# Kernel optimization log

Measured on AMD Instinct MI355X. Metric: run time of the kernel, lower is better.

Reference implementation:

```python
import jax, jax.numpy as jnp
import numpy as np

EPS = 1e-8


def l2norm(x, axis):
    # matches torch: x / (sqrt(sum(x^2)) + eps)
    return x / (jnp.sqrt(jnp.sum(x * x, axis=axis, keepdims=True)) + EPS)


def setup_inputs() -> dict:
    key = jax.random.key(0)
    k1, k2, k3, k4, k5 = jax.random.split(key, 5)
    I, C, L, R, D = 16, 32, 32, 36, 1024  # n_image, n_caption, max_words, n_regions, embed_dim
    img_emb = l2norm(jax.random.normal(k1, (I, R, D), jnp.float32), -1)
    cap_emb = l2norm(jax.random.normal(k2, (C, L, D), jnp.float32), -1)
    W_emb = jax.random.normal(k3, (D, D), jnp.float32)  # nn.Embedding weight, N(0,1) default init
    sim_map_w = 2.5 + 0.1 * jax.random.normal(k4, (1, D), jnp.float32)  # init_weight: normal(2.5, 0.1)
    temp_scale_w = jnp.full((1, 1), np.log(1.0 / 0.07), jnp.float32)    # init_weight
    temp_learnable_w = jnp.full((1, 1), 4.0, jnp.float32)               # init_weight
    cap_lens = jax.random.randint(k5, (C,), 4, L + 1, jnp.int32)        # ragged caption lengths in [4, L]
    return dict(img_emb=img_emb, cap_emb=cap_emb, W_emb=W_emb, sim_map_w=sim_map_w,
                temp_scale_w=temp_scale_w, temp_learnable_w=temp_learnable_w, cap_lens=cap_lens)


def reference(img_emb, cap_emb, W_emb, sim_map_w, temp_scale_w, temp_learnable_w, cap_lens):
    D = W_emb.shape[0]
    L = cap_emb.shape[1]
    # --- dimension-weight branch (caption-independent) ---
    # linspace(0, D, D).long(): last index is D (out of range in torch); gather with clip.
    idx = jnp.floor(jnp.linspace(0.0, D, D)).astype(jnp.int32)
    weights = jax.nn.sigmoid(jnp.take(W_emb, idx, axis=0, mode='clip'))  # (D, D)
    mean_p = jnp.mean(weights, axis=1)                  # (D,)
    std_p = jnp.std(weights, axis=1, ddof=1)            # torch.std is unbiased
    thres = mean_p + sim_map_w[0] * std_p               # (D,)
    values = jnp.exp(temp_learnable_w[0, 0]) * (weights - thres[:, None])
    mask_p = jnp.tanh(jnp.exp(values))
    Dlw = l2norm(mask_p * weights, axis=1)              # Dim_learned_weights (D, D)
    diag = Dlw.sum(0)                                   # Diagonal (D,); diag_embed matmul == elementwise scale
    smooth = jnp.exp(temp_scale_w[0, 0])
    # --- vectorized ragged per-caption cross attention ---
    wmask = (jnp.arange(L)[None, :] < cap_lens[:, None]).astype(cap_emb.dtype)  # (C, L)
    # attn[c,i,l,r] = tanh(sum_d cap[c,l,d] * diag[d] * img[i,r,d])
    attn = jnp.tanh(jnp.einsum('cld,ird->cilr', cap_emb, img_emb * diag))
    attn = jnp.where(attn >= 0, attn, 0.1 * attn) * wmask[:, None, :, None]  # LeakyReLU(0.1), zero padded words
    attn = attn / (jnp.sqrt(jnp.sum(attn * attn, axis=2, keepdims=True)) + EPS)  # l2norm over word dim
    attn = jax.nn.softmax(attn * smooth, axis=3)        # softmax over regions
    ctx = l2norm(jnp.einsum('cilr,ird->cild', attn, img_emb), axis=-1)  # Context_img
    sim_loc = ctx * cap_emb[:, None, :, :]
    sim_sub = jnp.einsum('cild,ed->cile', sim_loc, Dlw)  # sim_loc @ Dlw.T
    sim_vec = l2norm(sim_sub, axis=-1).sum(-1)           # (C, I, L)
    # mean over the n_word valid words of each caption
    sim = jnp.sum(sim_vec * wmask[:, None, :], axis=2) / cap_lens[:, None].astype(cap_emb.dtype)  # (C, I)
    return sim.T  # (n_image, n_caption), matching torch.cat(sim_all, 1)
```

## Files before the change

kernel.cpp:

```cpp
#include <hip/hip_runtime.h>
#include <hip/hip_bf16.h>

#define I_N 16
#define C_N 32
#define L_N 32
#define R_N 36
#define D_N 1024
#define EPSF 1e-8f

typedef _Float16 f16;
typedef __attribute__((ext_vector_type(8))) _Float16 half8;
typedef __attribute__((ext_vector_type(4))) float floatx4;

__device__ __forceinline__ void gl16(const f16* g, f16* l) {
  __builtin_amdgcn_global_load_lds(
      (const __attribute__((address_space(1))) void*)g,
      (__attribute__((address_space(3))) void*)l, 16, 0, 0);
}

__device__ __forceinline__ float fast_tanh(float x) {
  float q = __expf(-2.f * fabsf(x));
  float t = (1.f - q) / (1.f + q);
  return (x >= 0.f) ? t : -t;
}

__device__ __forceinline__ float wave_sum64(float v) {
  #pragma unroll
  for (int off = 32; off > 0; off >>= 1) v += __shfl_xor(v, off, 64);
  return v;
}

__global__ __launch_bounds__(256) void k_dlw(const float* __restrict__ W,
    const float* __restrict__ simw, const float* __restrict__ tlw,
    const float* __restrict__ img,
    f16* __restrict__ DlwH, f16* __restrict__ imgP) {
  int gw = blockIdx.x * 4 + (threadIdx.x >> 6);
  int lane = threadIdx.x & 63;
  if (gw >= 1024) {
    int row = gw - 1024;
    int i = row / 48, r = row % 48;
    size_t dst = (size_t)row * D_N;
    #pragma unroll
    for (int q = 0; q < 4; ++q) {
      int col = lane * 4 + q * 256;
      f16 h4[4];
      if (r < R_N) {
        size_t src = ((size_t)i * R_N + r) * D_N;
        float4 v = *(const float4*)(img + src + col);
        h4[0] = (f16)v.x; h4[1] = (f16)v.y; h4[2] = (f16)v.z; h4[3] = (f16)v.w;
      } else {
        h4[0] = h4[1] = h4[2] = h4[3] = (f16)0.f;
      }
      *(float2*)(imgP + dst + col) = *(float2*)h4;
    }
    return;
  }
  int row = gw;
  const float* Wr = W + (size_t)row * D_N;
  float w[16]; float p = 0.f;
  #pragma unroll
  for (int q = 0; q < 4; ++q) {
    float4 v = *(const float4*)(Wr + lane * 4 + q * 256);
    w[q*4+0] = 1.f / (1.f + __expf(-v.x));
    w[q*4+1] = 1.f / (1.f + __expf(-v.y));
    w[q*4+2] = 1.f / (1.f + __expf(-v.z));
    w[q*4+3] = 1.f / (1.f + __expf(-v.w));
    p += w[q*4+0] + w[q*4+1] + w[q*4+2] + w[q*4+3];
  }
  float S = wave_sum64(p);
  float mean = S * (1.f / 1024.f);
  p = 0.f;
  #pragma unroll
  for (int k = 0; k < 16; ++k) { float d = w[k] - mean; p += d * d; }
  float S2 = wave_sum64(p);
  float stdv = sqrtf(S2 * (1.f / 1023.f));
  float thres = mean + simw[row] * stdv;
  float eT = __expf(tlw[0]);
  p = 0.f;
  #pragma unroll
  for (int k = 0; k < 16; ++k) {
    float y = __expf(eT * (w[k] - thres));
    float q2 = __expf(-2.f * y);
    float mp = (1.f - q2) / (1.f + q2);
    w[k] = mp * w[k];
    p += w[k] * w[k];
  }
  float S3 = wave_sum64(p);
  float inv = 1.f / (sqrtf(S3) + EPSF);
  #pragma unroll
  for (int q = 0; q < 4; ++q) {
    f16 h4[4];
    #pragma unroll
    for (int t = 0; t < 4; ++t) h4[t] = (f16)(w[q*4+t] * inv);
    *(float2*)(DlwH + (size_t)row * D_N + lane * 4 + q * 256) = *(float2*)h4;
  }
}

__global__ __launch_bounds__(256) void k_dpp(const f16* __restrict__ DlwH,
    const int* __restrict__ lens, float* __restrict__ dpart,
    int* __restrict__ pfx, int* __restrict__ mp) {
  int bid = blockIdx.x;
  if (bid < 64) {
    int p = bid >> 2;
    int col = (bid & 3) * 256 + threadIdx.x;
    float s = 0.f;
    #pragma unroll 8
    for (int r = p * 64; r < p * 64 + 64; ++r) s += (float)DlwH[(size_t)r * D_N + col];
    dpart[(size_t)p * D_N + col] = s;
  } else if (threadIdx.x < 64) {
    int l = threadIdx.x;
    int v = (l < 32) ? lens[l] : 0;
    int s = v;
    #pragma unroll
    for (int off = 1; off < 32; off <<= 1) {
      int t = __shfl_up(s, off, 64);
      if (l >= off) s += t;
    }
    if (l < 32) pfx[l] = s - v;
    if (l == 31) { pfx[32] = s; mp[0] = s * 16; }
  }
}

__global__ __launch_bounds__(256) void k_capd(const float* __restrict__ dpart,
    const float* __restrict__ cap, f16* __restrict__ capD) {
  __shared__ float dg[D_N];
  int tid = threadIdx.x;
  #pragma unroll
  for (int k = 0; k < 4; ++k) {
    int col = tid + k * 256;
    float s = 0.f;
    #pragma unroll
    for (int p = 0; p < 16; ++p) s += dpart[(size_t)p * D_N + col];
    dg[col] = s;
  }
  __syncthreads();
  #pragma unroll
  for (int rr = 0; rr < 4; ++rr) {
    size_t base = (size_t)(blockIdx.x * 4 + rr) * D_N;
    #pragma unroll
    for (int k = 0; k < 4; ++k) {
      int j = tid + k * 256;
      capD[base + j] = (f16)(cap[base + j] * dg[j]);
    }
  }
}

__global__ __launch_bounds__(256) void k_qk(const f16* __restrict__ A,
    const f16* __restrict__ B, const int* __restrict__ lens,
    const float* __restrict__ tsw, float* __restrict__ pw) {
  int mt = blockIdx.x;
  int i  = blockIdx.y;
  int tid = threadIdx.x;
  int w = tid >> 6, lane = tid & 63;
  int l15 = lane & 15, h = lane >> 4;
  __shared__ __align__(16) f16 Abuf[3][64 * 32];
  __shared__ __align__(16) f16 Bbuf[3][64 * 32];
  __shared__ float att[64][49];
  __shared__ float cn[2][R_N];
  floatx4 acc[3];
  #pragma unroll
  for (int nf = 0; nf < 3; ++nf) acc[nf] = (floatx4)0.f;

  int r_p = lane >> 2, u_p = lane & 3;
  int sw = (r_p >> 1) & 7;
  int val = (u_p | ((r_p & 1) << 2)) ^ sw;
  int r_l = (r_p & 14) | (val >> 2);
  int u_l = val & 3;
  const f16* Ag = A + (size_t)(mt * 64 + w * 16 + r_l) * D_N + u_l * 8;
  const f16* Bg = B + (size_t)(i * 48 + w * 16 + r_l) * D_N + u_l * 8;

  int v2 = (h | ((l15 & 1) << 2)) ^ ((l15 >> 1) & 7);
  int rbit = (v2 >> 2) & 1;
  int pun = (v2 & 3) * 8;
  int aoff = (w * 16 + (l15 & 14) + rbit) * 32 + pun;
  int boff[3];
  #pragma unroll
  for (int nf = 0; nf < 3; ++nf) boff[nf] = (nf * 16 + (l15 & 14) + rbit) * 32 + pun;

  #define QSTAGE(kt, b) { \
    int kof = (kt) * 32; \
    gl16(Ag + kof, &Abuf[b][(w * 16) * 32]); \
    gl16(Bg + kof, &Bbuf[b][(w * 16) * 32]); }
  #define QCOMPUTE(b) { \
    half8 a = *(const half8*)(&Abuf[b][aoff]); \
    _Pragma("unroll") for (int nf = 0; nf < 3; ++nf) { \
      half8 bb = *(const half8*)(&Bbuf[b][boff[nf]]); \
      acc[nf] = __builtin_amdgcn_mfma_f32_16x16x32_f16(a, bb, acc[nf], 0, 0, 0); } }

  QSTAGE(0, 0);
  QSTAGE(1, 1);
  int cur = 0, n2 = 2;
  for (int kk = 0; kk < 30; ++kk) {
    QSTAGE(kk + 2, n2);
    asm volatile("s_waitcnt vmcnt(4)" ::: "memory");
    __builtin_amdgcn_s_barrier();
    __builtin_amdgcn_sched_barrier(0);
    QCOMPUTE(cur);
    __builtin_amdgcn_s_barrier();
    cur = (cur == 2) ? 0 : cur + 1;
    n2  = (n2  == 2) ? 0 : n2  + 1;
  }
  asm volatile("s_waitcnt vmcnt(2)" ::: "memory");
  __builtin_amdgcn_s_barrier();
  __builtin_amdgcn_sched_barrier(0);
  QCOMPUTE(cur);
  __builtin_amdgcn_s_barrier();
  cur = (cur == 2) ? 0 : cur + 1;
  asm volatile("s_waitcnt vmcnt(0)" ::: "memory");
  __builtin_amdgcn_s_barrier();
  __builtin_amdgcn_sched_barrier(0);
  QCOMPUTE(cur);
  #undef QSTAGE
  #undef QCOMPUTE

  int len0 = lens[mt * 2], len1 = lens[mt * 2 + 1];
  #pragma unroll
  for (int nf = 0; nf < 3; ++nf)
    #pragma unroll
    for (int j = 0; j < 4; ++j) {
      int ml = w * 16 + h * 4 + j;
      int n = nf * 16 + l15;
      float t = fast_tanh(acc[nf][j]);
      float v = (t >= 0.f) ? t : 0.1f * t;
      int len = (ml >= 32) ? len1 : len0;
      if ((ml & 31) >= len || n >= R_N) v = 0.f;
      att[ml][n] = v;
    }
  __syncthreads();
  for (int e = tid; e < 2 * R_N; e += 256) {
    int cc = e / R_N, r = e % R_N;
    float s = 0.f;
    #pragma unroll
    for (int l = 0; l < 32; ++l) { float a = att[cc * 32 + l][r]; s += a * a; }
    cn[cc][r] = sqrtf(s) + EPSF;
  }
  __syncthreads();
  if (tid < 64) {
    int cc = tid >> 5, l = tid & 31;
    float smooth = __expf(tsw[0]);
    float mx = -3.4e38f;
    #pragma unroll
    for (int r = 0; r < R_N; ++r) {
      float z = att[tid][r] / cn[cc][r] * smooth;
      att[tid][r] = z;
      mx = fmaxf(mx, z);
    }
    float se = 0.f;
    #pragma unroll
    for (int r = 0; r < R_N; ++r) {
      float e2 = __expf(att[tid][r] - mx);
      att[tid][r] = e2;
      se += e2;
    }
    float inv = 1.f / se;
    float* dst = pw + ((size_t)i * 1024 + (mt * 2 + cc) * 32 + l) * R_N;
    #pragma unroll
    for (int r = 0; r < R_N; ++r) dst[r] = att[tid][r] * inv;
  }
}

__global__ __launch_bounds__(256) void k_ctx(const float* __restrict__ pw,
    const f16* __restrict__ imgP, const float* __restrict__ cap,
    const int* __restrict__ lens, const int* __restrict__ pfx,
    f16* __restrict__ slc) {
  int c  = blockIdx.x;
  int i  = blockIdx.y;
  int tid = threadIdx.x;
  int w = tid >> 6;
  int cg = tid & 63;
  int len = lens[c];
  int pf = pfx[c];
  __shared__ float pA[32][R_N];
  __shared__ __align__(16) f16 rows[R_N][1024];
  for (int e = tid; e < 32 * R_N; e += 256) {
    int rr = e / R_N, r = e % R_N;
    pA[rr][r] = pw[((size_t)i * 1024 + c * 32 + rr) * R_N + r];
  }
  const f16* base = imgP + (size_t)i * 48 * D_N;
  #pragma unroll
  for (int t = 0; t < 9; ++t) {
    int rr = w * 9 + t;
    const f16* src = base + (size_t)rr * D_N + cg * 8;
    gl16(src,       &rows[rr][0]);
    gl16(src + 512, &rows[rr][512]);
  }
  __syncthreads();
  int d0 = cg * 8, d1 = 512 + cg * 8;
  #pragma unroll
  for (int sub = 0; sub < 2; ++sub) {
    half8 acc0[4], acc1[4];
    #pragma unroll
    for (int j = 0; j < 4; ++j) { acc0[j] = (half8)(f16)0.f; acc1[j] = (half8)(f16)0.f; }
    for (int k = 0; k < R_N; ++k) {
      half8 h0 = *(const half8*)(&rows[k][d0]);
      half8 h1 = *(const half8*)(&rows[k][d1]);
      #pragma unroll
      for (int j = 0; j < 4; ++j) {
        f16 ah = (f16)pA[sub * 16 + w * 4 + j][k];
        acc0[j] = acc0[j] + h0 * ah;
        acc1[j] = acc1[j] + h1 * ah;
      }
    }
    #pragma unroll
    for (int j = 0; j < 4; ++j) {
      int l = sub * 16 + w * 4 + j;
      float af[16];
      #pragma unroll
      for (int q = 0; q < 8; ++q) { af[q] = (float)acc0[j][q]; af[8 + q] = (float)acc1[j][q]; }
      float ss = 0.f;
      #pragma unroll
      for (int q = 0; q < 16; ++q) ss += af[q] * af[q];
      #pragma unroll
      for (int off = 1; off < 64; off <<= 1) ss += __shfl_xor(ss, off, 64);
      if (l < len) {
        float inv = 1.f / (sqrtf(ss) + EPSF);
        const float* capr = cap + ((size_t)c * L_N + l) * D_N;
        float4 c0 = *(const float4*)(capr + d0);
        float4 c1 = *(const float4*)(capr + d0 + 4);
        float4 c2 = *(const float4*)(capr + d1);
        float4 c3 = *(const float4*)(capr + d1 + 4);
        float cv[16] = {c0.x,c0.y,c0.z,c0.w, c1.x,c1.y,c1.z,c1.w,
                        c2.x,c2.y,c2.z,c2.w, c3.x,c3.y,c3.z,c3.w};
        union { f16 h[16]; float4 f4[2]; } u;
        #pragma unroll
        for (int q = 0; q < 16; ++q) u.h[q] = (f16)(af[q] * inv * cv[q]);
        f16* dst = slc + ((size_t)((pf + l) * 16 + i)) * D_N;
        *(float4*)(dst + d0) = u.f4[0];
        *(float4*)(dst + d1) = u.f4[1];
      }
    }
  }
}

__global__ __launch_bounds__(256) void k_gemm(const f16* __restrict__ A,
    const f16* __restrict__ B, const int* __restrict__ mp,
    float* __restrict__ rs16, float* __restrict__ rq16) {
  int bx = blockIdx.x, by = blockIdx.y;
  int Mp = mp[0];
  int m0 = bx * 128, n0 = by * 128;
  if (m0 >= Mp) return;
  int tid = threadIdx.x;
  int w = tid >> 6, lane = tid & 63;
  int l15 = lane & 15, h = lane >> 4;
  int wm = w >> 1, wn = w & 1;
  __shared__ __align__(16) f16 AB[3][2][128 * 32];
  floatx4 acc[4][4];
  #pragma unroll
  for (int mf = 0; mf < 4; ++mf)
    #pragma unroll
    for (int nf = 0; nf < 4; ++nf) acc[mf][nf] = (floatx4)0.f;

  int r_p = lane >> 2, u_p = lane & 3;
  int sw = (r_p >> 1) & 7;
  int val = (u_p | ((r_p & 1) << 2)) ^ sw;
  int r_l = (r_p & 14) | (val >> 2);
  int u_l = val & 3;
  const f16* As0 = A + (size_t)(m0 + w * 32 +  0 + r_l) * D_N + u_l * 8;
  const f16* As1 = A + (size_t)(m0 + w * 32 + 16 + r_l) * D_N + u_l * 8;
  const f16* Bs0 = B + (size_t)(n0 + w * 32 +  0 + r_l) * D_N + u_l * 8;
  const f16* Bs1 = B + (size_t)(n0 + w * 32 + 16 + r_l) * D_N + u_l * 8;

  int v2 = (h | ((l15 & 1) << 2)) ^ ((l15 >> 1) & 7);
  int rbit = (v2 >> 2) & 1;
  int pun = (v2 & 3) * 8;
  int aoff[4], boff[4];
  #pragma unroll
  for (int f = 0; f < 4; ++f) {
    aoff[f] = (wm * 64 + f * 16 + (l15 & 14) + rbit) * 32 + pun;
    boff[f] = (wn * 64 + f * 16 + (l15 & 14) + rbit) * 32 + pun;
  }

  #define STAGE(kt, b) { \
    int kof = (kt) * 32; \
    gl16(As0 + kof, &AB[b][0][(w * 32 +  0) * 32]); \
    gl16(As1 + kof, &AB[b][0][(w * 32 + 16) * 32]); \
    gl16(Bs0 + kof, &AB[b][1][(w * 32 +  0) * 32]); \
    gl16(Bs1 + kof, &AB[b][1][(w * 32 + 16) * 32]); }

  #define COMPUTE(b) { \
    half8 af[4], bf[4]; \
    _Pragma("unroll") for (int f = 0; f < 4; ++f) af[f] = *(const half8*)(&AB[b][0][aoff[f]]); \
    _Pragma("unroll") for (int f = 0; f < 4; ++f) bf[f] = *(const half8*)(&AB[b][1][boff[f]]); \
    _Pragma("unroll") for (int mf = 0; mf < 4; ++mf) \
      _Pragma("unroll") for (int nf = 0; nf < 4; ++nf) \
        acc[mf][nf] = __builtin_amdgcn_mfma_f32_16x16x32_f16(af[mf], bf[nf], acc[mf][nf], 0, 0, 0); }

  STAGE(0, 0);
  STAGE(1, 1);
  int cur = 0, n2 = 2;
  for (int kk = 0; kk < 30; ++kk) {
    STAGE(kk + 2, n2);
    asm volatile("s_waitcnt vmcnt(8)" ::: "memory");
    __builtin_amdgcn_s_barrier();
    __builtin_amdgcn_sched_barrier(0);
    COMPUTE(cur);
    __builtin_amdgcn_s_barrier();
    cur = (cur == 2) ? 0 : cur + 1;
    n2  = (n2  == 2) ? 0 : n2  + 1;
  }
  asm volatile("s_waitcnt vmcnt(4)" ::: "memory");
  __builtin_amdgcn_s_barrier();
  __builtin_amdgcn_sched_barrier(0);
  COMPUTE(cur);
  __builtin_amdgcn_s_barrier();
  cur = (cur == 2) ? 0 : cur + 1;
  asm volatile("s_waitcnt vmcnt(0)" ::: "memory");
  __builtin_amdgcn_s_barrier();
  __builtin_amdgcn_sched_barrier(0);
  COMPUTE(cur);
  #undef STAGE
  #undef COMPUTE

  int slot = by * 2 + wn;
  #pragma unroll
  for (int mf = 0; mf < 4; ++mf)
    #pragma unroll
    for (int j = 0; j < 4; ++j) {
      float s = 0.f, q = 0.f;
      #pragma unroll
      for (int nf = 0; nf < 4; ++nf) { float v = acc[mf][nf][j]; s += v; q += v * v; }
      #pragma unroll
      for (int off = 1; off < 16; off <<= 1) { s += __shfl_xor(s, off, 64); q += __shfl_xor(q, off, 64); }
      if (l15 == 0) {
        int m = m0 + wm * 64 + mf * 16 + h * 4 + j;
        rs16[(size_t)slot * 16384 + m] = s;
        rq16[(size_t)slot * 16384 + m] = q;
      }
    }
}

__global__ __launch_bounds__(64) void k_final(const float* __restrict__ rs16,
    const float* __restrict__ rq16, const int* __restrict__ lens,
    const int* __restrict__ pfx, float* __restrict__ out) {
  int b = blockIdx.x;
  int c = b & 31;
  int l = threadIdx.x;
  int len = lens[c];
  float sv = 0.f;
  if (l < len) {
    int i = b >> 5;
    int row = (pfx[c] + l) * 16 + i;
    float rs = 0.f, rq = 0.f;
    #pragma unroll
    for (int s = 0; s < 16; ++s) {
      rs += rs16[(size_t)s * 16384 + row];
      rq += rq16[(size_t)s * 16384 + row];
    }
    sv = rs / (sqrtf(rq) + EPSF);
  }
  #pragma unroll
  for (int off = 32; off > 0; off >>= 1) sv += __shfl_down(sv, off, 64);
  if (l == 0) out[b] = sv / (float)len;
}

extern "C" void kernel_launch(void* const* d_in, const int* in_sizes, int n_in,
                              void* d_out, int out_size, void* d_ws, size_t ws_size,
                              hipStream_t stream) {
  const float* img  = (const float*)d_in[0];
  const float* cap  = (const float*)d_in[1];
  const float* W    = (const float*)d_in[2];
  const float* simw = (const float*)d_in[3];
  const float* tsw  = (const float*)d_in[4];
  const float* tlw  = (const float*)d_in[5];
  const int*   lens = (const int*)d_in[6];
  float* out = (float*)d_out;

  char* wsB = (char*)d_ws;
  if (ws_size < 51122176) return;
  f16*   DlwH  = (f16*)  (wsB + 4194304);
  f16*   capD  = (f16*)  (wsB + 6295552);
  f16*   imgP  = (f16*)  (wsB + 8392704);
  float* dpart = (float*)(wsB + 9965568);
  int*   mp    = (int*)  (wsB + 10031104);
  int*   pfx   = (int*)  (wsB + 10031360);
  float* pw    = (float*)(wsB + 13111296);
  f16*   slc   = (f16*)  (wsB + 15470592);
  float* rs16  = (float*)(wsB + 49025024);
  float* rq16  = (float*)(wsB + 50073600);

  k_dlw<<<448, 256, 0, stream>>>(W, simw, tlw, img, DlwH, imgP);
  k_dpp<<<65, 256, 0, stream>>>(DlwH, lens, dpart, pfx, mp);
  k_capd<<<256, 256, 0, stream>>>(dpart, cap, capD);
  k_qk<<<dim3(16, 16), 256, 0, stream>>>(capD, imgP, lens, tsw, pw);
  k_ctx<<<dim3(32, 16), 256, 0, stream>>>(pw, imgP, cap, lens, pfx, slc);
  k_gemm<<<dim3(128, 8), 256, 0, stream>>>(slc, DlwH, mp, rs16, rq16);
  k_final<<<512, 64, 0, stream>>>(rs16, rq16, lens, pfx, out);
}
```

Before: 89.57 us.

## Fuse attention-score kernel with context aggregation kernel

Merges the QK/softmax kernel and the context kernel into one, so the softmax probabilities stay in shared memory instead of going through a global buffer, and one kernel launch is removed. The image rows are prefetched into LDS right after the QK main loop, overlapping with the tanh/norm/softmax epilogue. The tradeoff is fewer blocks (256 instead of 512 for the context part), each doing two captions serially, plus a much larger LDS footprint (about 72KB rows plus the existing buffers), which may reduce occupancy.

```diff
diff --git a/kernel.cpp b/kernel.cpp
--- a/kernel.cpp
+++ b/kernel.cpp
@@ -145,9 +145,10 @@
   }
 }
 
-__global__ __launch_bounds__(256) void k_qk(const f16* __restrict__ A,
-    const f16* __restrict__ B, const int* __restrict__ lens,
-    const float* __restrict__ tsw, float* __restrict__ pw) {
+__global__ __launch_bounds__(256) void k_qkctx(const f16* __restrict__ A,
+    const f16* __restrict__ B, const float* __restrict__ cap,
+    const int* __restrict__ lens, const int* __restrict__ pfx,
+    const float* __restrict__ tsw, f16* __restrict__ slc) {
   int mt = blockIdx.x;
   int i  = blockIdx.y;
   int tid = threadIdx.x;
@@ -157,6 +158,7 @@
   __shared__ __align__(16) f16 Bbuf[3][64 * 32];
   __shared__ float att[64][49];
   __shared__ float cn[2][R_N];
+  __shared__ __align__(16) f16 rows[R_N][1024];
   floatx4 acc[3];
   #pragma unroll
   for (int nf = 0; nf < 3; ++nf) acc[nf] = (floatx4)0.f;
@@ -213,6 +215,18 @@
   #undef QSTAGE
   #undef QCOMPUTE
 
+  {
+    const f16* base = B + (size_t)i * 48 * D_N;
+    int cg = lane;
+    #pragma unroll
+    for (int t = 0; t < 9; ++t) {
+      int rr = w * 9 + t;
+      const f16* src = base + (size_t)rr * D_N + cg * 8;
+      gl16(src,       &rows[rr][0]);
+      gl16(src + 512, &rows[rr][512]);
+    }
+  }
+
   int len0 = lens[mt * 2], len1 = lens[mt * 2 + 1];
   #pragma unroll
   for (int nf = 0; nf < 3; ++nf)
@@ -236,7 +250,7 @@
   }
   __syncthreads();
   if (tid < 64) {
-    int cc = tid >> 5, l = tid & 31;
+    int cc = tid >> 5;
     float smooth = __expf(tsw[0]);
     float mx = -3.4e38f;
     #pragma unroll
@@ -253,80 +267,60 @@
       se += e2;
     }
     float inv = 1.f / se;
-    float* dst = pw + ((size_t)i * 1024 + (mt * 2 + cc) * 32 + l) * R_N;
-    #pragma unroll
-    for (int r = 0; r < R_N; ++r) dst[r] = att[tid][r] * inv;
-  }
-}
-
-__global__ __launch_bounds__(256) void k_ctx(const float* __restrict__ pw,
-    const f16* __restrict__ imgP, const float* __restrict__ cap,
-    const int* __restrict__ lens, const int* __restrict__ pfx,
-    f16* __restrict__ slc) {
-  int c  = blockIdx.x;
-  int i  = blockIdx.y;
-  int tid = threadIdx.x;
-  int w = tid >> 6;
-  int cg = tid & 63;
-  int len = lens[c];
-  int pf = pfx[c];
-  __shared__ float pA[32][R_N];
-  __shared__ __align__(16) f16 rows[R_N][1024];
-  for (int e = tid; e < 32 * R_N; e += 256) {
-    int rr = e / R_N, r = e % R_N;
-    pA[rr][r] = pw[((size_t)i * 1024 + c * 32 + rr) * R_N + r];
-  }
-  const f16* base = imgP + (size_t)i * 48 * D_N;
-  #pragma unroll
-  for (int t = 0; t < 9; ++t) {
-    int rr = w * 9 + t;
-    const f16* src = base + (size_t)rr * D_N + cg * 8;
-    gl16(src,       &rows[rr][0]);
-    gl16(src + 512, &rows[rr][512]);
+    #pragma unroll
+    for (int r = 0; r < R_N; ++r) att[tid][r] *= inv;
   }
   __syncthreads();
+
+  int cg = lane;
   int d0 = cg * 8, d1 = 512 + cg * 8;
   #pragma unroll
-  for (int sub = 0; sub < 2; ++sub) {
-    half8 acc0[4], acc1[4];
-    #pragma unroll
-    for (int j = 0; j < 4; ++j) { acc0[j] = (half8)(f16)0.f; acc1[j] = (half8)(f16)0.f; }
-    for (int k = 0; k < R_N; ++k) {
-      half8 h0 = *(const half8*)(&rows[k][d0]);
-      half8 h1 = *(const half8*)(&rows[k][d1]);
+  for (int cc = 0; cc < 2; ++cc) {
+    int c = mt * 2 + cc;
+    int len = (cc ? len1 : len0);
+    int pf = pfx[c];
+    #pragma unroll
+    for (int sub = 0; sub < 2; ++sub) {
+      half8 acc0[4], acc1[4];
+      #pragma unroll
+      for (int j = 0; j < 4; ++j) { acc0[j] = (half8)(f16)0.f; acc1[j] = (half8)(f16)0.f; }
+      for (int k = 0; k < R_N; ++k) {
+        half8 h0 = *(const half8*)(&rows[k][d0]);
+        half8 h1 = *(const half8*)(&rows[k][d1]);
+        #pragma unroll
+        for (int j = 0; j < 4; ++j) {
+          f16 ah = (f16)att[cc * 32 + sub * 16 + w * 4 + j][k];
+          acc0[j] = acc0[j] + h0 * ah;
+          acc1[j] = acc1[j] + h1 * ah;
+        }
+      }
       #pragma unroll
       for (int j = 0; j < 4; ++j) {
-        f16 ah = (f16)pA[sub * 16 + w * 4 + j][k];
-        acc0[j] = acc0[j] + h0 * ah;
-        acc1[j] = acc1[j] + h1 * ah;
-      }
-    }
-    #pragma unroll
-    for (int j = 0; j < 4; ++j) {
-      int l = sub * 16 + w * 4 + j;
-      float af[16];
-      #pragma unroll
-      for (int q = 0; q < 8; ++q) { af[q] = (float)acc0[j][q]; af[8 + q] = (float)acc1[j][q]; }
-      float ss = 0.f;
-      #pragma unroll
-      for (int q = 0; q < 16; ++q) ss += af[q] * af[q];
-      #pragma unroll
-      for (int off = 1; off < 64; off <<= 1) ss += __shfl_xor(ss, off, 64);
-      if (l < len) {
-        float inv = 1.f / (sqrtf(ss) + EPSF);
-        const float* capr = cap + ((size_t)c * L_N + l) * D_N;
-        float4 c0 = *(const float4*)(capr + d0);
-        float4 c1 = *(const float4*)(capr + d0 + 4);
-        float4 c2 = *(const float4*)(capr + d1);
-        float4 c3 = *(const float4*)(capr + d1 + 4);
-        float cv[16] = {c0.x,c0.y,c0.z,c0.w, c1.x,c1.y,c1.z,c1.w,
-                        c2.x,c2.y,c2.z,c2.w, c3.x,c3.y,c3.z,c3.w};
-        union { f16 h[16]; float4 f4[2]; } u;
+        int l = sub * 16 + w * 4 + j;
+        float af[16];
         #pragma unroll
-        for (int q = 0; q < 16; ++q) u.h[q] = (f16)(af[q] * inv * cv[q]);
-        f16* dst = slc + ((size_t)((pf + l) * 16 + i)) * D_N;
-        *(float4*)(dst + d0) = u.f4[0];
-        *(float4*)(dst + d1) = u.f4[1];
+        for (int q = 0; q < 8; ++q) { af[q] = (float)acc0[j][q]; af[8 + q] = (float)acc1[j][q]; }
+        float ss = 0.f;
+        #pragma unroll
+        for (int q = 0; q < 16; ++q) ss += af[q] * af[q];
+        #pragma unroll
+        for (int off = 1; off < 64; off <<= 1) ss += __shfl_xor(ss, off, 64);
+        if (l < len) {
+          float inv = 1.f / (sqrtf(ss) + EPSF);
+          const float* capr = cap + ((size_t)c * L_N + l) * D_N;
+          float4 c0 = *(const float4*)(capr + d0);
+          float4 c1 = *(const float4*)(capr + d0 + 4);
+          float4 c2 = *(const float4*)(capr + d1);
+          float4 c3 = *(const float4*)(capr + d1 + 4);
+          float cv[16] = {c0.x,c0.y,c0.z,c0.w, c1.x,c1.y,c1.z,c1.w,
+                          c2.x,c2.y,c2.z,c2.w, c3.x,c3.y,c3.z,c3.w};
+          union { f16 hh[16]; float4 f4[2]; } u;
+          #pragma unroll
+          for (int q = 0; q < 16; ++q) u.hh[q] = (f16)(af[q] * inv * cv[q]);
+          f16* dst = slc + ((size_t)((pf + l) * 16 + i)) * D_N;
+          *(float4*)(dst + d0) = u.f4[0];
+          *(float4*)(dst + d1) = u.f4[1];
+        }
       }
     }
   }
@@ -473,7 +467,6 @@
   float* dpart = (float*)(wsB + 9965568);
   int*   mp    = (int*)  (wsB + 10031104);
   int*   pfx   = (int*)  (wsB + 10031360);
-  float* pw    = (float*)(wsB + 13111296);
   f16*   slc   = (f16*)  (wsB + 15470592);
   float* rs16  = (float*)(wsB + 49025024);
   float* rq16  = (float*)(wsB + 50073600);
@@ -481,8 +474,7 @@
   k_dlw<<<448, 256, 0, stream>>>(W, simw, tlw, img, DlwH, imgP);
   k_dpp<<<65, 256, 0, stream>>>(DlwH, lens, dpart, pfx, mp);
   k_capd<<<256, 256, 0, stream>>>(dpart, cap, capD);
-  k_qk<<<dim3(16, 16), 256, 0, stream>>>(capD, imgP, lens, tsw, pw);
-  k_ctx<<<dim3(32, 16), 256, 0, stream>>>(pw, imgP, cap, lens, pfx, slc);
+  k_qkctx<<<dim3(16, 16), 256, 0, stream>>>(capD, imgP, cap, lens, pfx, tsw, slc);
   k_gemm<<<dim3(128, 8), 256, 0, stream>>>(slc, DlwH, mp, rs16, rq16);
   k_final<<<512, 64, 0, stream>>>(rs16, rq16, lens, pfx, out);
 }
```

After: 92.08 us (median of 2 runs). 2.8% more time.
